# Kernel optimization log

Measured on AMD Instinct MI355X. Metric: run time of the kernel, lower is better.

The kernel has to match this reference:

```python
import jax, jax.numpy as jnp
import numpy as np

EPS = 1e-5
COORD_TAU, COORD_KAPPA = 1.0, 1.0
COT_TAU, COT_LAM = 0.8, 0.7
GATE_FLOOR = 0.05


def _gconv(x, w, b=None):
    # grouped 1x1 conv: x [B,C,H,W], w [g, co_per_g, ci_per_g]
    B, C, H, W = x.shape
    g, co, ci = w.shape
    y = jnp.einsum('goi,bgihw->bgohw', w, x.reshape(B, g, ci, H, W)).reshape(B, g * co, H, W)
    return y if b is None else y + b[None, :, None, None]


def _conv1x1(x, w):
    # dense 1x1 conv: w [Cout, Cin]
    return jnp.einsum('oi,bihw->bohw', w, x)


def _inorm(x, g, b):
    # InstanceNorm2d(affine=True): per (B,C) stats over spatial dims, biased var
    mu = x.mean(axis=(2, 3), keepdims=True)
    var = x.var(axis=(2, 3), keepdims=True)
    return (x - mu) * jax.lax.rsqrt(var + EPS) * g[None, :, None, None] + b[None, :, None, None]


def _axis_softmax(z, L, axis):
    # stabilized softmax along a spatial axis, mean-rescaled by L
    zz = z / COORD_TAU
    zz = zz - zz.max(axis=axis, keepdims=True)
    return jax.nn.softmax(zz, axis=axis) * L


def _forward(x, compress_w, inc_g, inc_b, coord_proj_w, coord_proj_g, coord_proj_b,
             coord_h_w, coord_h_b, coord_wc_w, coord_wc_b, coord_alpha, coord_beta,
             cot_key_w, cot_val_w, cot_att1_w, cot_attn_g, cot_attn_b, cot_att2_w,
             cot_fuse_w, fusion_w, fus_g, fus_b, gate_w, expand_w):
    xc = jax.nn.relu(_inorm(_conv1x1(x, compress_w), inc_g, inc_b))  # [B,m,H,W]
    B, C, H, W = xc.shape

    # ---- Coord2H branch (use_softmax=True path) ----
    def proj(t):
        return jax.nn.silu(_inorm(_gconv(t, coord_proj_w), coord_proj_g, coord_proj_b))

    zh = _gconv(proj(xc.mean(axis=3, keepdims=True)), coord_h_w, coord_h_b)   # [B,C,H,1]
    zw = _gconv(proj(xc.mean(axis=2, keepdims=True)), coord_wc_w, coord_wc_b)  # [B,C,1,W]
    ah = _axis_softmax(zh, H, 2)
    aw = _axis_softmax(zw, W, 3)
    w_lin = coord_alpha * ah + coord_beta * aw  # broadcasts to [B,C,H,W]
    coord_out = xc * (1.0 + COORD_KAPPA * (w_lin - 1.0))

    # ---- CoT branch ----
    k1 = _gconv(xc, cot_key_w)
    v = _gconv(xc, cot_val_w)
    y = jnp.concatenate([k1, xc], axis=1)  # [B,2C,H,W]
    att = jax.nn.relu(_inorm(_gconv(y, cot_att1_w), cot_attn_g, cot_attn_b))
    att_logits = _gconv(att, cot_att2_w)
    z = (att_logits / COT_TAU).reshape(B, C, H * W)
    sm = jax.nn.softmax(z - z.max(axis=-1, keepdims=True), axis=-1).reshape(B, C, H, W) * (H * W)
    att_mix = (1.0 - COT_LAM) * jax.nn.sigmoid(att_logits) + COT_LAM * sm
    cot_out = _conv1x1(k1 + att_mix * v, cot_fuse_w)

    # ---- fusion + gate + expand ----
    fused = jax.nn.relu(_inorm(_conv1x1(jnp.concatenate([coord_out, cot_out], axis=1), fusion_w), fus_g, fus_b))
    gate = jax.nn.sigmoid(jnp.einsum('oi,bi->bo', gate_w, fused.mean(axis=(2, 3))))[:, :, None, None]  # [B,1,1,1]
    return _conv1x1(fused * (gate * (1.0 - GATE_FLOOR) + GATE_FLOOR), expand_w)


def setup_inputs() -> dict:
    key = jax.random.key(0)
    B, DIM, H, W = 8, 512, 128, 128
    RED, G = 16, 4
    m = DIM // RED  # 32
    mg = m // G     # 8
    ks = jax.random.split(key, 23)

    def n(k, s, sc=0.05):
        return jax.random.normal(k, s, dtype=jnp.float32) * sc

    return {
        'x': jax.random.normal(ks[0], (B, DIM, H, W), dtype=jnp.float32),
        'compress_w': n(ks[1], (m, DIM)),
        'inc_g': 1.0 + n(ks[2], (m,)),
        'inc_b': n(ks[3], (m,)),
        'coord_proj_w': n(ks[4], (G, mg, mg), 0.2),
        'coord_proj_g': 1.0 + n(ks[5], (m,)),
        'coord_proj_b': n(ks[6], (m,)),
        'coord_h_w': n(ks[7], (G, mg, mg), 0.2),
        'coord_h_b': n(ks[8], (m,)),
        'coord_wc_w': n(ks[9], (G, mg, mg), 0.2),
        'coord_wc_b': n(ks[10], (m,)),
        'coord_alpha': jnp.asarray(0.5, dtype=jnp.float32),
        'coord_beta': jnp.asarray(0.5, dtype=jnp.float32),
        'cot_key_w': n(ks[11], (G, mg, mg), 0.2),
        'cot_val_w': n(ks[12], (G, mg, mg), 0.2),
        'cot_att1_w': n(ks[13], (G, mg, 2 * mg), 0.2),
        'cot_attn_g': 1.0 + n(ks[14], (m,)),
        'cot_attn_b': n(ks[15], (m,)),
        'cot_att2_w': n(ks[16], (G, mg, mg), 0.2),
        'cot_fuse_w': n(ks[17], (m, m), 0.1),
        'fusion_w': n(ks[18], (m, 2 * m), 0.1),
        'fus_g': 1.0 + n(ks[19], (m,)),
        'fus_b': n(ks[20], (m,)),
        'gate_w': n(ks[21], (1, m), 0.2),
        'expand_w': n(ks[22], (DIM, m), 0.1),
    }


def reference(x, compress_w, inc_g, inc_b, coord_proj_w, coord_proj_g, coord_proj_b,
              coord_h_w, coord_h_b, coord_wc_w, coord_wc_b, coord_alpha, coord_beta,
              cot_key_w, cot_val_w, cot_att1_w, cot_attn_g, cot_attn_b, cot_att2_w,
              cot_fuse_w, fusion_w, fus_g, fus_b, gate_w, expand_w):
    return _forward(x, compress_w, inc_g, inc_b, coord_proj_w, coord_proj_g, coord_proj_b,
                    coord_h_w, coord_h_b, coord_wc_w, coord_wc_b, coord_alpha, coord_beta,
                    cot_key_w, cot_val_w, cot_att1_w, cot_attn_g, cot_attn_b, cot_att2_w,
                    cot_fuse_w, fusion_w, fus_g, fus_b, gate_w, expand_w)
```

## Files before the change

### kernel.cpp

```cpp
#include <hip/hip_runtime.h>
#include <math.h>

#define NB 8
#define CIN 512
#define CM 32
#define MG 8
#define HH 128
#define WW 128
#define HWSZ (HH*WW)
#define EPSF 1e-5f
#define COT_ITAU 1.25f
#define LAM 0.7f
#define GFLOOR 0.05f

typedef float vf4 __attribute__((ext_vector_type(4)));

__device__ __forceinline__ float wsum(float v){
#pragma unroll
  for (int o = 32; o; o >>= 1) v += __shfl_xor(v, o, 64);
  return v;
}

__global__ void k_tw(const float* __restrict__ w, float* __restrict__ wT){
  int i = blockIdx.x*256 + threadIdx.x;
  if (i < CM*CIN){
    int c = i >> 9, k = i & (CIN-1);
    wT[k*CM + c] = w[i];
  }
}

__global__ __launch_bounds__(256) void k_compress(
    const float* __restrict__ x, const float* __restrict__ wT,
    float* __restrict__ y, float* __restrict__ s1, float* __restrict__ s2)
{
  int tid = threadIdx.x;
  int b = blockIdx.x >> 6;
  int p = ((blockIdx.x & 63) << 8) + tid;
  const float* xb = x + ((size_t)b*CIN)*HWSZ + p;
  float acc[CM];
#pragma unroll
  for (int c=0;c<CM;c++) acc[c]=0.f;
  float xv[8], xn[8];
#pragma unroll
  for (int u=0;u<8;u++) xv[u] = __builtin_nontemporal_load(&xb[(size_t)u*HWSZ]);
  for (int i=0;i<CIN;i+=8){
    if (i+8<CIN){
#pragma unroll
      for (int u=0;u<8;u++) xn[u] = __builtin_nontemporal_load(&xb[(size_t)(i+8+u)*HWSZ]);
    }
#pragma unroll
    for (int u=0;u<8;u++){
      const float* wr = wT + (i+u)*CM;
#pragma unroll
      for (int c=0;c<CM;c++) acc[c]=fmaf(wr[c],xv[u],acc[c]);
    }
#pragma unroll
    for (int u=0;u<8;u++) xv[u]=xn[u];
  }
  float* yb = y + ((size_t)b*CM)*HWSZ + p;
#pragma unroll
  for (int c=0;c<CM;c++) yb[(size_t)c*HWSZ] = acc[c];
  float ms=0.f, mq=0.f;
#pragma unroll
  for (int c=0;c<CM;c++){
    float s = wsum(acc[c]);
    float q = wsum(acc[c]*acc[c]);
    if ((tid&63)==c){ ms=s; mq=q; }
  }
  int lane = tid & 63;
  if (lane < CM){
    atomicAdd(&s1[b*CM+lane], ms);
    atomicAdd(&s2[b*CM+lane], mq);
  }
}

__global__ __launch_bounds__(256) void k_poolstat(
  const float* __restrict__ y,
  const float* __restrict__ s1i, const float* __restrict__ s2i,
  const float* __restrict__ incg, const float* __restrict__ incb,
  const float* __restrict__ kw, const float* __restrict__ a1w,
  float* __restrict__ s1, float* __restrict__ s2,
  float* __restrict__ hpool, float* __restrict__ wpart)
{
  __shared__ float nA[CM], nB[CM];
  __shared__ float sh[CM][128];
  int tid=threadIdx.x;
  int blk=blockIdx.x;
  int b = blk >> 6;
  int p = ((blk&63)<<8)+tid;
  if (tid<CM){
    float mu  = s1i[b*CM+tid]*(1.f/HWSZ);
    float var = fmaf(-mu,mu, s2i[b*CM+tid]*(1.f/HWSZ));
    float a   = rsqrtf(var+EPSF)*incg[tid];
    nA[tid]=a; nB[tid]=incb[tid]-mu*a;
  }
  __syncthreads();
  size_t base = ((size_t)b*CM)*HWSZ + p;
  float xc[CM], k1[CM], at[CM];
#pragma unroll
  for (int c=0;c<CM;c++)
    xc[c] = fmaxf(0.f, fmaf(y[base+(size_t)c*HWSZ], nA[c], nB[c]));
  if (tid>=128){
#pragma unroll
    for (int c=0;c<CM;c++) sh[c][tid-128]=xc[c];
  }
  __syncthreads();
  if (tid<128){
    float* wp = wpart + (size_t)blk*(CM*WW) + tid;
#pragma unroll
    for (int c=0;c<CM;c++) wp[c*WW] = xc[c] + sh[c][tid];
  }
  {
    int hrow = p >> 7;
    float ms=0.f;
#pragma unroll
    for (int c=0;c<CM;c++){
      float s=wsum(xc[c]);
      if ((tid&63)==c) ms=s;
    }
    int lane=tid&63;
    if (lane<CM) atomicAdd(&hpool[(b*CM+lane)*HH+hrow], ms*(1.f/WW));
  }
#pragma unroll
  for (int gI=0;gI<4;gI++)
#pragma unroll
    for (int o=0;o<MG;o++){
      float sk=0.f;
#pragma unroll
      for (int i=0;i<MG;i++) sk = fmaf(kw[gI*64+o*8+i], xc[gI*MG+i], sk);
      k1[gI*MG+o]=sk;
    }
#pragma unroll
  for (int gI=0;gI<4;gI++)
#pragma unroll
    for (int o=0;o<MG;o++){
      float s=0.f;
#pragma unroll
      for (int i=0;i<16;i++){
        float inp = (gI<2) ? k1[gI*16+i] : xc[(gI-2)*16+i];
        s = fmaf(a1w[gI*128+o*16+i], inp, s);
      }
      at[gI*MG+o]=s;
    }
  float ms=0.f,mq=0.f;
#pragma unroll
  for (int c=0;c<CM;c++){
    float s=wsum(at[c]); float q=wsum(at[c]*at[c]);
    if ((tid&63)==c){ms=s;mq=q;}
  }
  int lane=tid&63;
  if (lane<CM){ atomicAdd(&s1[b*CM+lane],ms); atomicAdd(&s2[b*CM+lane],mq); }
}

__global__ __launch_bounds__(256) void k_cot2(
  const float* __restrict__ y,
  const float* __restrict__ s1i, const float* __restrict__ s2i,
  const float* __restrict__ incg, const float* __restrict__ incb,
  const float* __restrict__ s1a, const float* __restrict__ s2a,
  const float* __restrict__ ag, const float* __restrict__ ab,
  const float* __restrict__ kw, const float* __restrict__ a1w, const float* __restrict__ a2w,
  const float* __restrict__ hpool, const float* __restrict__ wpart,
  const float* __restrict__ pjw, const float* __restrict__ pjg, const float* __restrict__ pjb,
  const float* __restrict__ chw, const float* __restrict__ chb,
  const float* __restrict__ cww, const float* __restrict__ cwb,
  float* __restrict__ es, float* __restrict__ ah, float* __restrict__ aw)
{
  __shared__ float T[CM][HH+1];
  __shared__ float sa[CM], sb[CM], smx[CM], ssc[CM];
  __shared__ float nA[CM], nB[CM], tA[CM], tB[CM];
  int tid=threadIdx.x;
  int blk=blockIdx.x;
  int b = blk >> 6;
  int p = ((blk&63)<<8)+tid;
  if (tid<CM){
    float mu  = s1i[b*CM+tid]*(1.f/HWSZ);
    float var = fmaf(-mu,mu, s2i[b*CM+tid]*(1.f/HWSZ));
    float a   = rsqrtf(var+EPSF)*incg[tid];
    nA[tid]=a; nB[tid]=incb[tid]-mu*a;
    float mu2  = s1a[b*CM+tid]*(1.f/HWSZ);
    float var2 = fmaf(-mu2,mu2, s2a[b*CM+tid]*(1.f/HWSZ));
    float a2   = rsqrtf(var2+EPSF)*ag[tid];
    tA[tid]=a2; tB[tid]=ab[tid]-mu2*a2;
  }
  __syncthreads();
  size_t base = ((size_t)b*CM)*HWSZ + p;
  float xc[CM], k1[CM], at[CM], l[CM];
#pragma unroll
  for (int c=0;c<CM;c++)
    xc[c] = fmaxf(0.f, fmaf(y[base+(size_t)c*HWSZ], nA[c], nB[c]));
#pragma unroll
  for (int gI=0;gI<4;gI++)
#pragma unroll
    for (int o=0;o<MG;o++){
      float sk=0.f;
#pragma unroll
      for (int i=0;i<MG;i++) sk = fmaf(kw[gI*64+o*8+i], xc[gI*MG+i], sk);
      k1[gI*MG+o]=sk;
    }
#pragma unroll
  for (int gI=0;gI<4;gI++)
#pragma unroll
    for (int o=0;o<MG;o++){
      float s=0.f;
#pragma unroll
      for (int i=0;i<16;i++){
        float inp = (gI<2) ? k1[gI*16+i] : xc[(gI-2)*16+i];
        s = fmaf(a1w[gI*128+o*16+i], inp, s);
      }
      at[gI*MG+o]=s;
    }
#pragma unroll
  for (int c=0;c<CM;c++)
    at[c] = fmaxf(0.f, fmaf(at[c], tA[c], tB[c]));
#pragma unroll
  for (int gI=0;gI<4;gI++)
#pragma unroll
    for (int o=0;o<MG;o++){
      float s=0.f;
#pragma unroll
      for (int i=0;i<MG;i++) s = fmaf(a2w[gI*64+o*8+i], at[gI*8+i], s);
      l[gI*MG+o]=s;
    }
  float ms=0.f;
#pragma unroll
  for (int c=0;c<CM;c++){
    float s = wsum(__expf(l[c]*COT_ITAU));
    if ((tid&63)==c) ms=s;
  }
  int lane=tid&63;
  if (lane<CM) atomicAdd(&es[b*CM+lane], ms);

  if (blk < 2*NB){
    int bb = blk>>1, path = blk&1;
    const float* w2 = path ? cww : chw;
    const float* b2 = path ? cwb : chb;
    float* outp     = path ? aw  : ah;
    float in[CM];
    if (path==1){
      __syncthreads();
      for (int t=tid; t<CM*WW; t+=256){
        const float* src = wpart + (size_t)(bb*64)*(CM*WW) + t;
        float s=0.f;
#pragma unroll 8
        for (int k=0;k<64;k++) s += src[(size_t)k*(CM*WW)];
        T[t>>7][t&127] = s*(1.f/HH);
      }
      __syncthreads();
      if (tid<HH){
#pragma unroll
        for (int c=0;c<CM;c++) in[c]=T[c][tid];
      }
      __syncthreads();
    } else {
      if (tid<HH){
#pragma unroll
        for (int c=0;c<CM;c++) in[c]=hpool[(bb*CM+c)*HH+tid];
      }
      __syncthreads();
    }
    if (tid<HH){
#pragma unroll
      for (int gI=0;gI<4;gI++)
#pragma unroll
        for (int o=0;o<MG;o++){
          float s=0.f;
#pragma unroll
          for (int i=0;i<MG;i++) s = fmaf(pjw[gI*64+o*8+i], in[gI*8+i], s);
          T[gI*8+o][tid] = s;
        }
    }
    __syncthreads();
    if (tid < CM){
      float s=0.f, q=0.f;
      for (int k=0;k<HH;k++){ float t=T[tid][k]; s+=t; q+=t*t; }
      float mu = s*(1.0f/HH);
      float var = q*(1.0f/HH) - mu*mu;
      float a = rsqrtf(var+EPSF)*pjg[tid];
      sa[tid]=a; sb[tid]=pjb[tid]-mu*a;
    }
    __syncthreads();
    float z[CM];
    if (tid<HH){
      float sil[CM];
#pragma unroll
      for (int c=0;c<CM;c++){
        float val = fmaf(T[c][tid], sa[c], sb[c]);
        sil[c] = val/(1.f+__expf(-val));
      }
#pragma unroll
      for (int gI=0;gI<4;gI++)
#pragma unroll
        for (int o=0;o<MG;o++){
          float s=b2[gI*8+o];
#pragma unroll
          for (int i=0;i<MG;i++) s = fmaf(w2[gI*64+o*8+i], sil[gI*8+i], s);
          z[gI*8+o]=s;
        }
    }
    __syncthreads();
    if (tid<HH){
#pragma unroll
      for (int c=0;c<CM;c++) T[c][tid]=z[c];
    }
    __syncthreads();
    if (tid < CM){
      float mx=-1e30f;
      for (int k=0;k<HH;k++) mx = fmaxf(mx, T[tid][k]);
      float s=0.f;
      for (int k=0;k<HH;k++) s += __expf(T[tid][k]-mx);
      smx[tid]=mx; ssc[tid]=(float)HH/s;
    }
    __syncthreads();
    if (tid<HH){
#pragma unroll
      for (int c=0;c<CM;c++)
        outp[(bb*CM+c)*HH + tid] = __expf(T[c][tid]-smx[c])*ssc[c];
    }
  }
}

__global__ __launch_bounds__(256) void k_mix_fuse(
  const float* __restrict__ y,
  const float* __restrict__ s1i, const float* __restrict__ s2i,
  const float* __restrict__ incg, const float* __restrict__ incb,
  const float* __restrict__ s1a, const float* __restrict__ s2a,
  const float* __restrict__ ag, const float* __restrict__ ab,
  const float* __restrict__ kw, const float* __restrict__ vw,
  const float* __restrict__ a1w, const float* __restrict__ a2w,
  const float* __restrict__ ah, const float* __restrict__ awp, const float* __restrict__ es,
  const float* __restrict__ alpha, const float* __restrict__ beta,
  const float* __restrict__ fw, const float* __restrict__ fuw,
  float* __restrict__ fpo, float* __restrict__ s1, float* __restrict__ s2)
{
  __shared__ float nA[CM], nB[CM], tA[CM], tB[CM];
  int tid=threadIdx.x;
  int b = blockIdx.x>>6;
  int p = ((blockIdx.x&63)<<8)+tid;
  int h = p >> 7, w = p & (WW-1);
  if (tid<CM){
    float mu  = s1i[b*CM+tid]*(1.f/HWSZ);
    float var = fmaf(-mu,mu, s2i[b*CM+tid]*(1.f/HWSZ));
    float a   = rsqrtf(var+EPSF)*incg[tid];
    nA[tid]=a; nB[tid]=incb[tid]-mu*a;
    float mu2  = s1a[b*CM+tid]*(1.f/HWSZ);
    float var2 = fmaf(-mu2,mu2, s2a[b*CM+tid]*(1.f/HWSZ));
    float a2   = rsqrtf(var2+EPSF)*ag[tid];
    tA[tid]=a2; tB[tid]=ab[tid]-mu2*a2;
  }
  __syncthreads();
  size_t base = ((size_t)b*CM)*HWSZ + p;
  float al=alpha[0], be=beta[0];
  float xc[CM], k1[CM], at[CM], l[CM], t[CM];
#pragma unroll
  for (int c=0;c<CM;c++)
    xc[c] = fmaxf(0.f, fmaf(y[base+(size_t)c*HWSZ], nA[c], nB[c]));
#pragma unroll
  for (int gI=0;gI<4;gI++)
#pragma unroll
    for (int o=0;o<MG;o++){
      float sk=0.f;
#pragma unroll
      for (int i=0;i<MG;i++) sk = fmaf(kw[gI*64+o*8+i], xc[gI*MG+i], sk);
      k1[gI*MG+o]=sk;
    }
#pragma unroll
  for (int gI=0;gI<4;gI++)
#pragma unroll
    for (int o=0;o<MG;o++){
      float s=0.f;
#pragma unroll
      for (int i=0;i<16;i++){
        float inp = (gI<2) ? k1[gI*16+i] : xc[(gI-2)*16+i];
        s = fmaf(a1w[gI*128+o*16+i], inp, s);
      }
      at[gI*MG+o]=s;
    }
#pragma unroll
  for (int c=0;c<CM;c++)
    at[c] = fmaxf(0.f, fmaf(at[c], tA[c], tB[c]));
#pragma unroll
  for (int gI=0;gI<4;gI++)
#pragma unroll
    for (int o=0;o<MG;o++){
      float s=0.f;
#pragma unroll
      for (int i=0;i<MG;i++) s = fmaf(a2w[gI*64+o*8+i], at[gI*8+i], s);
      l[gI*MG+o]=s;
    }
#pragma unroll
  for (int gI=0;gI<4;gI++)
#pragma unroll
    for (int o=0;o<MG;o++){
      float sv=0.f;
#pragma unroll
      for (int i=0;i<MG;i++) sv = fmaf(vw[gI*64+o*8+i], xc[gI*MG+i], sv);
      int c = gI*MG+o;
      float lgv = l[c];
      float sm = __expf(lgv*COT_ITAU) * (16384.f/es[b*CM+c]);
      float sg = 1.f/(1.f+__expf(-lgv));
      float mix = (1.f-LAM)*sg + LAM*sm;
      t[c] = fmaf(mix, sv, k1[c]);
    }
  float co[CM];
#pragma unroll
  for (int c=0;c<CM;c++){
    float wl = al*ah[(b*CM+c)*HH + h] + be*awp[(b*CM+c)*WW + w];
    co[c] = xc[c] * wl;
  }
  float cot[CM];
#pragma unroll
  for (int o=0;o<CM;o++){
    float s=0.f;
#pragma unroll
    for (int i=0;i<CM;i++) s = fmaf(fw[o*CM+i], t[i], s);
    cot[o]=s;
  }
  float ms=0.f, mq=0.f;
#pragma unroll
  for (int o=0;o<CM;o++){
    float s=0.f;
#pragma unroll
    for (int i=0;i<CM;i++) s = fmaf(fuw[o*64+i], co[i], s);
#pragma unroll
    for (int i=0;i<CM;i++) s = fmaf(fuw[o*64+32+i], cot[i], s);
    fpo[base+(size_t)o*HWSZ]=s;
    float ss = wsum(s); float qq = wsum(s*s);
    if ((tid&63)==o){ ms=ss; mq=qq; }
  }
  int lane=tid&63;
  if (lane<CM){ atomicAdd(&s1[b*CM+lane],ms); atomicAdd(&s2[b*CM+lane],mq); }
}

__global__ __launch_bounds__(256) void k_gstat(const float4* __restrict__ fp,
  const float* __restrict__ s1f, const float* __restrict__ s2f,
  const float* __restrict__ fg, const float* __restrict__ fb,
  float* __restrict__ gsum)
{
  int idx = blockIdx.x*256+threadIdx.x;
  int bc = idx >> 12;
  int c = bc & (CM-1);
  float mu  = s1f[bc]*(1.f/HWSZ);
  float var = fmaf(-mu,mu, s2f[bc]*(1.f/HWSZ));
  float a   = rsqrtf(var+EPSF)*fg[c];
  float bb  = fb[c]-mu*a;
  float4 tv = fp[idx];
  float s = fmaxf(0.f,fmaf(tv.x,a,bb))+fmaxf(0.f,fmaf(tv.y,a,bb))
          + fmaxf(0.f,fmaf(tv.z,a,bb))+fmaxf(0.f,fmaf(tv.w,a,bb));
  s = wsum(s);
  if ((threadIdx.x&63)==0) atomicAdd(&gsum[bc], s);
}

__global__ __launch_bounds__(256) void k_expand(const float4* __restrict__ fp4,
  const float* __restrict__ s1f, const float* __restrict__ s2f,
  const float* __restrict__ fg, const float* __restrict__ fb,
  const float* __restrict__ gw, const float* __restrict__ gsum,
  const float* __restrict__ ew, vf4* __restrict__ out4)
{
  __shared__ float fA[CM], fB[CM];
  int tid = threadIdx.x;
  int b = blockIdx.x >> 4;
  int tile = blockIdx.x & 15;
  int p4 = tile*256 + tid;
  int og = blockIdx.y * 64;
  if (tid<CM){
    float mu  = s1f[b*CM+tid]*(1.f/HWSZ);
    float var = fmaf(-mu,mu, s2f[b*CM+tid]*(1.f/HWSZ));
    float a   = rsqrtf(var+EPSF)*fg[tid];
    fA[tid]=a; fB[tid]=fb[tid]-mu*a;
  }
  float s=0.f;
#pragma unroll
  for (int c=0;c<CM;c++) s = fmaf(gw[c], gsum[b*CM+c], s);
  s *= (1.0f/HWSZ);
  float gt = 1.f/(1.f+__expf(-s));
  float sc = gt*(1.f-GFLOOR)+GFLOOR;
  __syncthreads();
  float4 f[CM];
  const float4* fbp = fp4 + ((size_t)b*CM)*(HWSZ/4) + p4;
#pragma unroll
  for (int c=0;c<CM;c++){
    float4 t = fbp[(size_t)c*(HWSZ/4)];
    float a=fA[c], bb=fB[c];
    f[c].x = fmaxf(0.f, fmaf(t.x,a,bb))*sc;
    f[c].y = fmaxf(0.f, fmaf(t.y,a,bb))*sc;
    f[c].z = fmaxf(0.f, fmaf(t.z,a,bb))*sc;
    f[c].w = fmaxf(0.f, fmaf(t.w,a,bb))*sc;
  }
  vf4* ob = out4 + ((size_t)b*CIN + og)*(HWSZ/4) + p4;
  for (int j=0;j<64;j++){
    const float* wr = ew + (og+j)*CM;
    vf4 acc = (vf4)(0.f);
#pragma unroll
    for (int c=0;c<CM;c++){
      float wv = wr[c];
      acc.x = fmaf(wv, f[c].x, acc.x);
      acc.y = fmaf(wv, f[c].y, acc.y);
      acc.z = fmaf(wv, f[c].z, acc.z);
      acc.w = fmaf(wv, f[c].w, acc.w);
    }
    __builtin_nontemporal_store(acc, &ob[(size_t)j*(HWSZ/4)]);
  }
}

extern "C" void kernel_launch(void* const* d_in, const int* in_sizes, int n_in,
                              void* d_out, int out_size, void* d_ws, size_t ws_size,
                              hipStream_t stream)
{
  const float* x    = (const float*)d_in[0];
  const float* cw   = (const float*)d_in[1];
  const float* incg = (const float*)d_in[2];
  const float* incb = (const float*)d_in[3];
  const float* pjw  = (const float*)d_in[4];
  const float* pjg  = (const float*)d_in[5];
  const float* pjb  = (const float*)d_in[6];
  const float* chw  = (const float*)d_in[7];
  const float* chb  = (const float*)d_in[8];
  const float* cww  = (const float*)d_in[9];
  const float* cwb  = (const float*)d_in[10];
  const float* alpha= (const float*)d_in[11];
  const float* beta = (const float*)d_in[12];
  const float* kw   = (const float*)d_in[13];
  const float* vw   = (const float*)d_in[14];
  const float* a1w  = (const float*)d_in[15];
  const float* ag   = (const float*)d_in[16];
  const float* ab   = (const float*)d_in[17];
  const float* a2w  = (const float*)d_in[18];
  const float* fw   = (const float*)d_in[19];
  const float* fuw  = (const float*)d_in[20];
  const float* fg   = (const float*)d_in[21];
  const float* fb   = (const float*)d_in[22];
  const float* gw   = (const float*)d_in[23];
  const float* ew   = (const float*)d_in[24];
  float* out = (float*)d_out;

  float* ws = (float*)d_ws;
  const size_t BIG = (size_t)NB*CM*HWSZ;
  float* y    = ws;
  float* F    = ws +   BIG;
  float* sm   = ws + 2*BIG;
  float* acc   = sm;  sm += 2048;
  float* statS = acc,      *statQ = acc+256;
  float* attS  = acc+512,  *attQ  = acc+768;
  float* esum  = acc+1024;
  float* fusS  = acc+1280, *fusQ  = acc+1536;
  float* gsum  = acc+1792;
  float* hpool = sm;  sm += NB*CM*HH;
  float* wT    = sm;  sm += CM*CIN;
  float* wpart = sm;  sm += (size_t)512*CM*WW;
  float* ahB   = sm;  sm += NB*CM*HH;
  float* awB   = sm;  sm += NB*CM*WW;

  hipMemsetAsync(acc, 0, (2048 + NB*CM*HH)*sizeof(float), stream);
  k_tw<<<64,256,0,stream>>>(cw, wT);
  k_compress<<<512,256,0,stream>>>(x, wT, y, statS, statQ);
  k_poolstat<<<512,256,0,stream>>>(y,statS,statQ,incg,incb,kw,a1w,attS,attQ,hpool,wpart);
  k_cot2<<<512,256,0,stream>>>(y,statS,statQ,incg,incb,attS,attQ,ag,ab,kw,a1w,a2w,
                               hpool,wpart,pjw,pjg,pjb,chw,chb,cww,cwb,esum,ahB,awB);
  k_mix_fuse<<<512,256,0,stream>>>(y,statS,statQ,incg,incb,attS,attQ,ag,ab,kw,vw,a1w,a2w,
                                   ahB,awB,esum,alpha,beta,fw,fuw,F,fusS,fusQ);
  k_gstat<<<4096,256,0,stream>>>((const float4*)F,fusS,fusQ,fg,fb,gsum);
  k_expand<<<dim3(128,8),256,0,stream>>>((const float4*)F,fusS,fusQ,fg,fb,gw,gsum,ew,(vf4*)out);
}
```

Baseline: 397.6 us.

## Split compress GEMM over input-channel groups with vectorized loads and separate reductions

The compress 1x1 conv is split into four input-channel groups (512 blocks in a 2D grid), each thread handling four pixels with float4 loads and writing partial sums to a workspace. A separate combine kernel sums the partials, writes y and accumulates the instance-norm statistics. The width-pool reduction is moved out of the two k_cot2 blocks into its own kernel. This aims for more memory-level parallelism and wider loads, at the cost of writing and re-reading four full-size partial tensors and two extra launches.

```diff
diff --git a/kernel.cpp b/kernel.cpp
--- a/kernel.cpp
+++ b/kernel.cpp
@@ -29,49 +29,61 @@
   }
 }
 
-__global__ __launch_bounds__(256) void k_compress(
+__global__ __launch_bounds__(256) void k_compress4(
     const float* __restrict__ x, const float* __restrict__ wT,
-    float* __restrict__ y, float* __restrict__ s1, float* __restrict__ s2)
+    float* __restrict__ part)
 {
   int tid = threadIdx.x;
-  int b = blockIdx.x >> 6;
-  int p = ((blockIdx.x & 63) << 8) + tid;
-  const float* xb = x + ((size_t)b*CIN)*HWSZ + p;
-  float acc[CM];
-#pragma unroll
-  for (int c=0;c<CM;c++) acc[c]=0.f;
-  float xv[8], xn[8];
-#pragma unroll
-  for (int u=0;u<8;u++) xv[u] = __builtin_nontemporal_load(&xb[(size_t)u*HWSZ]);
-  for (int i=0;i<CIN;i+=8){
-    if (i+8<CIN){
-#pragma unroll
-      for (int u=0;u<8;u++) xn[u] = __builtin_nontemporal_load(&xb[(size_t)(i+8+u)*HWSZ]);
-    }
-#pragma unroll
-    for (int u=0;u<8;u++){
-      const float* wr = wT + (i+u)*CM;
-#pragma unroll
-      for (int c=0;c<CM;c++) acc[c]=fmaf(wr[c],xv[u],acc[c]);
-    }
-#pragma unroll
-    for (int u=0;u<8;u++) xv[u]=xn[u];
-  }
-  float* yb = y + ((size_t)b*CM)*HWSZ + p;
-#pragma unroll
-  for (int c=0;c<CM;c++) yb[(size_t)c*HWSZ] = acc[c];
-  float ms=0.f, mq=0.f;
-#pragma unroll
-  for (int c=0;c<CM;c++){
-    float s = wsum(acc[c]);
-    float q = wsum(acc[c]*acc[c]);
-    if ((tid&63)==c){ ms=s; mq=q; }
-  }
-  int lane = tid & 63;
-  if (lane < CM){
-    atomicAdd(&s1[b*CM+lane], ms);
-    atomicAdd(&s2[b*CM+lane], mq);
-  }
+  int bt  = blockIdx.x;
+  int kg  = blockIdx.y;
+  int b   = bt >> 4;
+  int p4  = (bt & 15)*256 + tid;
+  const vf4* xb = (const vf4*)(x + ((size_t)b*CIN + kg*128)*HWSZ) + p4;
+  const float* wh = wT + kg*128*CM;
+  vf4 acc[CM];
+#pragma unroll
+  for (int c=0;c<CM;c++) acc[c] = (vf4)(0.f);
+  vf4 xv[4], xn[4];
+#pragma unroll
+  for (int u=0;u<4;u++) xv[u] = __builtin_nontemporal_load(xb + (size_t)u*(HWSZ/4));
+  for (int i=0;i<128;i+=4){
+    if (i+4<128){
+#pragma unroll
+      for (int u=0;u<4;u++) xn[u] = __builtin_nontemporal_load(xb + (size_t)(i+4+u)*(HWSZ/4));
+    }
+#pragma unroll
+    for (int u=0;u<4;u++){
+      const float* wr = wh + (i+u)*CM;
+#pragma unroll
+      for (int c=0;c<CM;c++){
+        float wv = wr[c];
+        acc[c].x = fmaf(wv, xv[u].x, acc[c].x);
+        acc[c].y = fmaf(wv, xv[u].y, acc[c].y);
+        acc[c].z = fmaf(wv, xv[u].z, acc[c].z);
+        acc[c].w = fmaf(wv, xv[u].w, acc[c].w);
+      }
+    }
+#pragma unroll
+    for (int u=0;u<4;u++) xv[u]=xn[u];
+  }
+  vf4* ob = (vf4*)(part + (size_t)kg*NB*CM*HWSZ) + (size_t)(b*CM)*(HWSZ/4) + p4;
+#pragma unroll
+  for (int c=0;c<CM;c++) ob[(size_t)c*(HWSZ/4)] = acc[c];
+}
+
+__global__ __launch_bounds__(256) void k_comb4(
+    const vf4* __restrict__ p0, const vf4* __restrict__ p1,
+    const vf4* __restrict__ p2, const vf4* __restrict__ p3,
+    vf4* __restrict__ y, float* __restrict__ s1, float* __restrict__ s2)
+{
+  int idx = blockIdx.x*256 + threadIdx.x;
+  vf4 a = p0[idx] + p1[idx] + p2[idx] + p3[idx];
+  y[idx] = a;
+  int bc = idx >> 12;
+  float s = a.x+a.y+a.z+a.w;
+  float q = a.x*a.x+a.y*a.y+a.z*a.z+a.w*a.w;
+  s = wsum(s); q = wsum(q);
+  if ((threadIdx.x&63)==0){ atomicAdd(&s1[bc],s); atomicAdd(&s2[bc],q); }
 }
 
 __global__ __launch_bounds__(256) void k_poolstat(
@@ -152,6 +164,18 @@
   if (lane<CM){ atomicAdd(&s1[b*CM+lane],ms); atomicAdd(&s2[b*CM+lane],mq); }
 }
 
+__global__ void k_wred(const float* __restrict__ wpart, float* __restrict__ wpool){
+  int bc = blockIdx.x;
+  int w  = threadIdx.x;
+  int b  = bc >> 5;
+  int c  = bc & 31;
+  const float* src = wpart + (size_t)(b*64)*(CM*WW) + c*WW + w;
+  float s=0.f;
+#pragma unroll 8
+  for (int k=0;k<64;k++) s += src[(size_t)k*(CM*WW)];
+  wpool[bc*WW + w] = s*(1.0f/HH);
+}
+
 __global__ __launch_bounds__(256) void k_cot2(
   const float* __restrict__ y,
   const float* __restrict__ s1i, const float* __restrict__ s2i,
@@ -159,7 +183,7 @@
   const float* __restrict__ s1a, const float* __restrict__ s2a,
   const float* __restrict__ ag, const float* __restrict__ ab,
   const float* __restrict__ kw, const float* __restrict__ a1w, const float* __restrict__ a2w,
-  const float* __restrict__ hpool, const float* __restrict__ wpart,
+  const float* __restrict__ hpool, const float* __restrict__ wpool,
   const float* __restrict__ pjw, const float* __restrict__ pjg, const float* __restrict__ pjb,
   const float* __restrict__ chw, const float* __restrict__ chb,
   const float* __restrict__ cww, const float* __restrict__ cwb,
@@ -232,33 +256,15 @@
 
   if (blk < 2*NB){
     int bb = blk>>1, path = blk&1;
-    const float* w2 = path ? cww : chw;
-    const float* b2 = path ? cwb : chb;
-    float* outp     = path ? aw  : ah;
-    float in[CM];
-    if (path==1){
-      __syncthreads();
-      for (int t=tid; t<CM*WW; t+=256){
-        const float* src = wpart + (size_t)(bb*64)*(CM*WW) + t;
-        float s=0.f;
-#pragma unroll 8
-        for (int k=0;k<64;k++) s += src[(size_t)k*(CM*WW)];
-        T[t>>7][t&127] = s*(1.f/HH);
-      }
-      __syncthreads();
-      if (tid<HH){
-#pragma unroll
-        for (int c=0;c<CM;c++) in[c]=T[c][tid];
-      }
-      __syncthreads();
-    } else {
-      if (tid<HH){
-#pragma unroll
-        for (int c=0;c<CM;c++) in[c]=hpool[(bb*CM+c)*HH+tid];
-      }
-      __syncthreads();
-    }
+    const float* pool = path ? wpool : hpool;
+    const float* w2   = path ? cww : chw;
+    const float* b2   = path ? cwb : chb;
+    float* outp       = path ? aw  : ah;
+    float z[CM];
     if (tid<HH){
+      float in[CM];
+#pragma unroll
+      for (int c=0;c<CM;c++) in[c] = pool[(bb*CM+c)*HH + tid];
 #pragma unroll
       for (int gI=0;gI<4;gI++)
 #pragma unroll
@@ -279,7 +285,6 @@
       sa[tid]=a; sb[tid]=pjb[tid]-mu*a;
     }
     __syncthreads();
-    float z[CM];
     if (tid<HH){
       float sil[CM];
 #pragma unroll
@@ -535,9 +540,10 @@
 
   float* ws = (float*)d_ws;
   const size_t BIG = (size_t)NB*CM*HWSZ;
-  float* y    = ws;
-  float* F    = ws +   BIG;
-  float* sm   = ws + 2*BIG;
+  float* part = ws;
+  float* F    = ws;
+  float* y    = ws + 4*BIG;
+  float* sm   = ws + 5*BIG;
   float* acc   = sm;  sm += 2048;
   float* statS = acc,      *statQ = acc+256;
   float* attS  = acc+512,  *attQ  = acc+768;
@@ -547,15 +553,20 @@
   float* hpool = sm;  sm += NB*CM*HH;
   float* wT    = sm;  sm += CM*CIN;
   float* wpart = sm;  sm += (size_t)512*CM*WW;
+  float* wpool = sm;  sm += NB*CM*WW;
   float* ahB   = sm;  sm += NB*CM*HH;
   float* awB   = sm;  sm += NB*CM*WW;
 
   hipMemsetAsync(acc, 0, (2048 + NB*CM*HH)*sizeof(float), stream);
   k_tw<<<64,256,0,stream>>>(cw, wT);
-  k_compress<<<512,256,0,stream>>>(x, wT, y, statS, statQ);
+  k_compress4<<<dim3(128,4),256,0,stream>>>(x, wT, part);
+  k_comb4<<<4096,256,0,stream>>>((const vf4*)part,(const vf4*)(part+BIG),
+                                 (const vf4*)(part+2*BIG),(const vf4*)(part+3*BIG),
+                                 (vf4*)y, statS, statQ);
   k_poolstat<<<512,256,0,stream>>>(y,statS,statQ,incg,incb,kw,a1w,attS,attQ,hpool,wpart);
+  k_wred<<<NB*CM,128,0,stream>>>(wpart, wpool);
   k_cot2<<<512,256,0,stream>>>(y,statS,statQ,incg,incb,attS,attQ,ag,ab,kw,a1w,a2w,
-                               hpool,wpart,pjw,pjg,pjb,chw,chb,cww,cwb,esum,ahB,awB);
+                               hpool,wpool,pjw,pjg,pjb,chw,chb,cww,cwb,esum,ahB,awB);
   k_mix_fuse<<<512,256,0,stream>>>(y,statS,statQ,incg,incb,attS,attQ,ag,ab,kw,vw,a1w,a2w,
                                    ahB,awB,esum,alpha,beta,fw,fuw,F,fusS,fusQ);
   k_gstat<<<4096,256,0,stream>>>((const float4*)F,fusS,fusQ,fg,fb,gsum);
```

Result: faster. 368.0 us (-7.5%).

## Stage compress input through double-buffered LDS and split W-pool reduction kernel

Applied to the files above, without the earlier changes.

The compress kernel now loads 32-channel slabs of x as float4 vectors into a double-buffered shared-memory tile, prefetching the next slab while computing. Results are also written back through LDS with vectorized stores. Separately, the W-axis pooling reduction moves out of two k_cot2 blocks into a dedicated small kernel, so those blocks no longer serialize a long reduction. This adds 64KB of LDS per block, which may lower occupancy, plus one extra launch.

```diff
diff --git a/kernel.cpp b/kernel.cpp
--- a/kernel.cpp
+++ b/kernel.cpp
@@ -33,44 +33,81 @@
     const float* __restrict__ x, const float* __restrict__ wT,
     float* __restrict__ y, float* __restrict__ s1, float* __restrict__ s2)
 {
+  __shared__ float lds[2][CM][256];
   int tid = threadIdx.x;
-  int b = blockIdx.x >> 6;
-  int p = ((blockIdx.x & 63) << 8) + tid;
-  const float* xb = x + ((size_t)b*CIN)*HWSZ + p;
+  int b   = blockIdx.x >> 6;
+  int tile0 = (blockIdx.x & 63) << 8;
+  const float* xb = x + ((size_t)b*CIN)*HWSZ + tile0;
+
+  {
+    const vf4* src = (const vf4*)xb;
+    vf4 tmp[8];
+#pragma unroll
+    for (int j=0;j<8;j++){
+      int f = tid + 256*j;
+      tmp[j] = __builtin_nontemporal_load(src + (size_t)(f>>6)*(HWSZ/4) + (f&63));
+    }
+#pragma unroll
+    for (int j=0;j<8;j++){
+      int f = tid + 256*j;
+      *((vf4*)&lds[0][f>>6][(f&63)*4]) = tmp[j];
+    }
+  }
   float acc[CM];
 #pragma unroll
   for (int c=0;c<CM;c++) acc[c]=0.f;
-  float xv[8], xn[8];
-#pragma unroll
-  for (int u=0;u<8;u++) xv[u] = __builtin_nontemporal_load(&xb[(size_t)u*HWSZ]);
-  for (int i=0;i<CIN;i+=8){
-    if (i+8<CIN){
-#pragma unroll
-      for (int u=0;u<8;u++) xn[u] = __builtin_nontemporal_load(&xb[(size_t)(i+8+u)*HWSZ]);
-    }
-#pragma unroll
-    for (int u=0;u<8;u++){
-      const float* wr = wT + (i+u)*CM;
-#pragma unroll
-      for (int c=0;c<CM;c++) acc[c]=fmaf(wr[c],xv[u],acc[c]);
-    }
-#pragma unroll
-    for (int u=0;u<8;u++) xv[u]=xn[u];
-  }
-  float* yb = y + ((size_t)b*CM)*HWSZ + p;
-#pragma unroll
-  for (int c=0;c<CM;c++) yb[(size_t)c*HWSZ] = acc[c];
-  float ms=0.f, mq=0.f;
-#pragma unroll
-  for (int c=0;c<CM;c++){
-    float s = wsum(acc[c]);
-    float q = wsum(acc[c]*acc[c]);
-    if ((tid&63)==c){ ms=s; mq=q; }
-  }
-  int lane = tid & 63;
-  if (lane < CM){
-    atomicAdd(&s1[b*CM+lane], ms);
-    atomicAdd(&s2[b*CM+lane], mq);
+
+  for (int t=0; t<16; ++t){
+    int cur = t & 1;
+    __syncthreads();
+    if (t+1 < 16){
+      const vf4* src = (const vf4*)(xb + (size_t)(t+1)*CM*HWSZ);
+      vf4 tmp[8];
+#pragma unroll
+      for (int j=0;j<8;j++){
+        int f = tid + 256*j;
+        tmp[j] = __builtin_nontemporal_load(src + (size_t)(f>>6)*(HWSZ/4) + (f&63));
+      }
+#pragma unroll
+      for (int j=0;j<8;j++){
+        int f = tid + 256*j;
+        *((vf4*)&lds[cur^1][f>>6][(f&63)*4]) = tmp[j];
+      }
+    }
+    const float* wr0 = wT + t*CM*CM;
+#pragma unroll
+    for (int i=0;i<CM;i++){
+      float xv = lds[cur][i][tid];
+      const float* wr = wr0 + i*CM;
+#pragma unroll
+      for (int c=0;c<CM;c++) acc[c] = fmaf(wr[c], xv, acc[c]);
+    }
+  }
+  {
+    float ms=0.f, mq=0.f;
+#pragma unroll
+    for (int c=0;c<CM;c++){
+      float s = wsum(acc[c]);
+      float q = wsum(acc[c]*acc[c]);
+      if ((tid&63)==c){ ms=s; mq=q; }
+    }
+    int lane = tid & 63;
+    if (lane < CM){
+      atomicAdd(&s1[b*CM+lane], ms);
+      atomicAdd(&s2[b*CM+lane], mq);
+    }
+  }
+  __syncthreads();
+#pragma unroll
+  for (int c=0;c<CM;c++) lds[0][c][tid] = acc[c];
+  __syncthreads();
+  {
+    vf4* yb = (vf4*)(y + ((size_t)b*CM)*HWSZ + tile0);
+#pragma unroll
+    for (int j=0;j<8;j++){
+      int f = tid + 256*j;
+      yb[(size_t)(f>>6)*(HWSZ/4) + (f&63)] = *((vf4*)&lds[0][f>>6][(f&63)*4]);
+    }
   }
 }
 
@@ -152,6 +189,18 @@
   if (lane<CM){ atomicAdd(&s1[b*CM+lane],ms); atomicAdd(&s2[b*CM+lane],mq); }
 }
 
+__global__ void k_wred(const float* __restrict__ wpart, float* __restrict__ wpool){
+  int bc = blockIdx.x;
+  int w  = threadIdx.x;
+  int b  = bc >> 5;
+  int c  = bc & 31;
+  const float* src = wpart + (size_t)(b*64)*(CM*WW) + c*WW + w;
+  float s=0.f;
+#pragma unroll 8
+  for (int k=0;k<64;k++) s += src[(size_t)k*(CM*WW)];
+  wpool[bc*WW + w] = s*(1.0f/HH);
+}
+
 __global__ __launch_bounds__(256) void k_cot2(
   const float* __restrict__ y,
   const float* __restrict__ s1i, const float* __restrict__ s2i,
@@ -159,7 +208,7 @@
   const float* __restrict__ s1a, const float* __restrict__ s2a,
   const float* __restrict__ ag, const float* __restrict__ ab,
   const float* __restrict__ kw, const float* __restrict__ a1w, const float* __restrict__ a2w,
-  const float* __restrict__ hpool, const float* __restrict__ wpart,
+  const float* __restrict__ hpool, const float* __restrict__ wpool,
   const float* __restrict__ pjw, const float* __restrict__ pjg, const float* __restrict__ pjb,
   const float* __restrict__ chw, const float* __restrict__ chb,
   const float* __restrict__ cww, const float* __restrict__ cwb,
@@ -232,33 +281,15 @@
 
   if (blk < 2*NB){
     int bb = blk>>1, path = blk&1;
-    const float* w2 = path ? cww : chw;
-    const float* b2 = path ? cwb : chb;
-    float* outp     = path ? aw  : ah;
-    float in[CM];
-    if (path==1){
-      __syncthreads();
-      for (int t=tid; t<CM*WW; t+=256){
-        const float* src = wpart + (size_t)(bb*64)*(CM*WW) + t;
-        float s=0.f;
-#pragma unroll 8
-        for (int k=0;k<64;k++) s += src[(size_t)k*(CM*WW)];
-        T[t>>7][t&127] = s*(1.f/HH);
-      }
-      __syncthreads();
-      if (tid<HH){
-#pragma unroll
-        for (int c=0;c<CM;c++) in[c]=T[c][tid];
-      }
-      __syncthreads();
-    } else {
-      if (tid<HH){
-#pragma unroll
-        for (int c=0;c<CM;c++) in[c]=hpool[(bb*CM+c)*HH+tid];
-      }
-      __syncthreads();
-    }
+    const float* pool = path ? wpool : hpool;
+    const float* w2   = path ? cww : chw;
+    const float* b2   = path ? cwb : chb;
+    float* outp       = path ? aw  : ah;
+    float z[CM];
     if (tid<HH){
+      float in[CM];
+#pragma unroll
+      for (int c=0;c<CM;c++) in[c] = pool[(bb*CM+c)*HH + tid];
 #pragma unroll
       for (int gI=0;gI<4;gI++)
 #pragma unroll
@@ -279,7 +310,6 @@
       sa[tid]=a; sb[tid]=pjb[tid]-mu*a;
     }
     __syncthreads();
-    float z[CM];
     if (tid<HH){
       float sil[CM];
 #pragma unroll
@@ -547,6 +577,7 @@
   float* hpool = sm;  sm += NB*CM*HH;
   float* wT    = sm;  sm += CM*CIN;
   float* wpart = sm;  sm += (size_t)512*CM*WW;
+  float* wpool = sm;  sm += NB*CM*WW;
   float* ahB   = sm;  sm += NB*CM*HH;
   float* awB   = sm;  sm += NB*CM*WW;
 
@@ -554,8 +585,9 @@
   k_tw<<<64,256,0,stream>>>(cw, wT);
   k_compress<<<512,256,0,stream>>>(x, wT, y, statS, statQ);
   k_poolstat<<<512,256,0,stream>>>(y,statS,statQ,incg,incb,kw,a1w,attS,attQ,hpool,wpart);
+  k_wred<<<NB*CM,128,0,stream>>>(wpart, wpool);
   k_cot2<<<512,256,0,stream>>>(y,statS,statQ,incg,incb,attS,attQ,ag,ab,kw,a1w,a2w,
-                               hpool,wpart,pjw,pjg,pjb,chw,chb,cww,cwb,esum,ahB,awB);
+                               hpool,wpool,pjw,pjg,pjb,chw,chb,cww,cwb,esum,ahB,awB);
   k_mix_fuse<<<512,256,0,stream>>>(y,statS,statQ,incg,incb,attS,attQ,ag,ab,kw,vw,a1w,a2w,
                                    ahB,awB,esum,alpha,beta,fw,fuw,F,fusS,fusQ);
   k_gstat<<<4096,256,0,stream>>>((const float4*)F,fusS,fusQ,fg,fb,gsum);
```

After: 376.8 us. 1.06x faster.

## Split compress reduction over four waves and move W-pool reduction to its own kernel

Applied to the files above, without the earlier changes.

The compress GEMM now gives each block a 64-pixel tile and splits the 512 input channels across four waves. Partial sums are reduced through shared memory, which quadruples the grid to 2048 blocks for better occupancy and latency hiding. Stores become vectorized float4 writes, and stats are reduced per channel. Separately, the W-direction pooling reduction that serially ran inside 8 blocks of k_cot2 is moved to a dedicated k_wred kernel with 256 blocks, removing a serial tail at the cost of an extra launch and workspace buffer.

```diff
diff --git a/kernel.cpp b/kernel.cpp
--- a/kernel.cpp
+++ b/kernel.cpp
@@ -33,44 +33,66 @@
     const float* __restrict__ x, const float* __restrict__ wT,
     float* __restrict__ y, float* __restrict__ s1, float* __restrict__ s2)
 {
-  int tid = threadIdx.x;
-  int b = blockIdx.x >> 6;
-  int p = ((blockIdx.x & 63) << 8) + tid;
-  const float* xb = x + ((size_t)b*CIN)*HWSZ + p;
+  __shared__ float part[4][CM][64];
+  int tid  = threadIdx.x;
+  int lane = tid & 63;
+  int g    = tid >> 6;
+  int blk  = blockIdx.x;
+  int b    = blk >> 8;
+  int tile0 = (blk & 255) << 6;
+  const float* xb = x + ((size_t)b*CIN + g*128)*HWSZ + tile0 + lane;
+  const float* wh = wT + (g*128)*CM;
+
   float acc[CM];
 #pragma unroll
   for (int c=0;c<CM;c++) acc[c]=0.f;
   float xv[8], xn[8];
 #pragma unroll
   for (int u=0;u<8;u++) xv[u] = __builtin_nontemporal_load(&xb[(size_t)u*HWSZ]);
-  for (int i=0;i<CIN;i+=8){
-    if (i+8<CIN){
+  for (int i=0;i<128;i+=8){
+    if (i+8<128){
 #pragma unroll
       for (int u=0;u<8;u++) xn[u] = __builtin_nontemporal_load(&xb[(size_t)(i+8+u)*HWSZ]);
     }
 #pragma unroll
     for (int u=0;u<8;u++){
-      const float* wr = wT + (i+u)*CM;
+      const float* wr = wh + (i+u)*CM;
 #pragma unroll
       for (int c=0;c<CM;c++) acc[c]=fmaf(wr[c],xv[u],acc[c]);
     }
 #pragma unroll
     for (int u=0;u<8;u++) xv[u]=xn[u];
   }
-  float* yb = y + ((size_t)b*CM)*HWSZ + p;
-#pragma unroll
-  for (int c=0;c<CM;c++) yb[(size_t)c*HWSZ] = acc[c];
-  float ms=0.f, mq=0.f;
-#pragma unroll
-  for (int c=0;c<CM;c++){
-    float s = wsum(acc[c]);
-    float q = wsum(acc[c]*acc[c]);
-    if ((tid&63)==c){ ms=s; mq=q; }
-  }
-  int lane = tid & 63;
-  if (lane < CM){
-    atomicAdd(&s1[b*CM+lane], ms);
-    atomicAdd(&s2[b*CM+lane], mq);
+#pragma unroll
+  for (int c=0;c<CM;c++) part[g][c][lane]=acc[c];
+  __syncthreads();
+  {
+    int idx0 = tid*8;
+    int c = idx0>>6, p0 = idx0&63;
+    vf4 a0 = *((vf4*)&part[0][c][p0])   + *((vf4*)&part[1][c][p0])
+           + *((vf4*)&part[2][c][p0])   + *((vf4*)&part[3][c][p0]);
+    vf4 a1 = *((vf4*)&part[0][c][p0+4]) + *((vf4*)&part[1][c][p0+4])
+           + *((vf4*)&part[2][c][p0+4]) + *((vf4*)&part[3][c][p0+4]);
+    *((vf4*)&part[0][c][p0])   = a0;
+    *((vf4*)&part[0][c][p0+4]) = a1;
+  }
+  __syncthreads();
+#pragma unroll
+  for (int cc=0;cc<8;cc++){
+    int c = g*8+cc;
+    float v = part[0][c][lane];
+    float s = wsum(v);
+    float q = wsum(v*v);
+    if (lane==0){
+      atomicAdd(&s1[b*CM+c], s);
+      atomicAdd(&s2[b*CM+c], q);
+    }
+  }
+#pragma unroll
+  for (int k=0;k<2;k++){
+    int s = tid + 256*k;
+    int c = s>>4, p4 = (s&15)*4;
+    *((vf4*)(y + ((size_t)(b*CM+c))*HWSZ + tile0 + p4)) = *((vf4*)&part[0][c][p4]);
   }
 }
 
@@ -152,6 +174,18 @@
   if (lane<CM){ atomicAdd(&s1[b*CM+lane],ms); atomicAdd(&s2[b*CM+lane],mq); }
 }
 
+__global__ void k_wred(const float* __restrict__ wpart, float* __restrict__ wpool){
+  int bc = blockIdx.x;
+  int w  = threadIdx.x;
+  int b  = bc >> 5;
+  int c  = bc & 31;
+  const float* src = wpart + (size_t)(b*64)*(CM*WW) + c*WW + w;
+  float s=0.f;
+#pragma unroll 8
+  for (int k=0;k<64;k++) s += src[(size_t)k*(CM*WW)];
+  wpool[bc*WW + w] = s*(1.0f/HH);
+}
+
 __global__ __launch_bounds__(256) void k_cot2(
   const float* __restrict__ y,
   const float* __restrict__ s1i, const float* __restrict__ s2i,
@@ -159,7 +193,7 @@
   const float* __restrict__ s1a, const float* __restrict__ s2a,
   const float* __restrict__ ag, const float* __restrict__ ab,
   const float* __restrict__ kw, const float* __restrict__ a1w, const float* __restrict__ a2w,
-  const float* __restrict__ hpool, const float* __restrict__ wpart,
+  const float* __restrict__ hpool, const float* __restrict__ wpool,
   const float* __restrict__ pjw, const float* __restrict__ pjg, const float* __restrict__ pjb,
   const float* __restrict__ chw, const float* __restrict__ chb,
   const float* __restrict__ cww, const float* __restrict__ cwb,
@@ -232,33 +266,15 @@
 
   if (blk < 2*NB){
     int bb = blk>>1, path = blk&1;
-    const float* w2 = path ? cww : chw;
-    const float* b2 = path ? cwb : chb;
-    float* outp     = path ? aw  : ah;
-    float in[CM];
-    if (path==1){
-      __syncthreads();
-      for (int t=tid; t<CM*WW; t+=256){
-        const float* src = wpart + (size_t)(bb*64)*(CM*WW) + t;
-        float s=0.f;
-#pragma unroll 8
-        for (int k=0;k<64;k++) s += src[(size_t)k*(CM*WW)];
-        T[t>>7][t&127] = s*(1.f/HH);
-      }
-      __syncthreads();
-      if (tid<HH){
-#pragma unroll
-        for (int c=0;c<CM;c++) in[c]=T[c][tid];
-      }
-      __syncthreads();
-    } else {
-      if (tid<HH){
-#pragma unroll
-        for (int c=0;c<CM;c++) in[c]=hpool[(bb*CM+c)*HH+tid];
-      }
-      __syncthreads();
-    }
+    const float* pool = path ? wpool : hpool;
+    const float* w2   = path ? cww : chw;
+    const float* b2   = path ? cwb : chb;
+    float* outp       = path ? aw  : ah;
+    float z[CM];
     if (tid<HH){
+      float in[CM];
+#pragma unroll
+      for (int c=0;c<CM;c++) in[c] = pool[(bb*CM+c)*HH + tid];
 #pragma unroll
       for (int gI=0;gI<4;gI++)
 #pragma unroll
@@ -279,7 +295,6 @@
       sa[tid]=a; sb[tid]=pjb[tid]-mu*a;
     }
     __syncthreads();
-    float z[CM];
     if (tid<HH){
       float sil[CM];
 #pragma unroll
@@ -547,15 +562,17 @@
   float* hpool = sm;  sm += NB*CM*HH;
   float* wT    = sm;  sm += CM*CIN;
   float* wpart = sm;  sm += (size_t)512*CM*WW;
+  float* wpool = sm;  sm += NB*CM*WW;
   float* ahB   = sm;  sm += NB*CM*HH;
   float* awB   = sm;  sm += NB*CM*WW;
 
   hipMemsetAsync(acc, 0, (2048 + NB*CM*HH)*sizeof(float), stream);
   k_tw<<<64,256,0,stream>>>(cw, wT);
-  k_compress<<<512,256,0,stream>>>(x, wT, y, statS, statQ);
+  k_compress<<<2048,256,0,stream>>>(x, wT, y, statS, statQ);
   k_poolstat<<<512,256,0,stream>>>(y,statS,statQ,incg,incb,kw,a1w,attS,attQ,hpool,wpart);
+  k_wred<<<NB*CM,128,0,stream>>>(wpart, wpool);
   k_cot2<<<512,256,0,stream>>>(y,statS,statQ,incg,incb,attS,attQ,ag,ab,kw,a1w,a2w,
-                               hpool,wpart,pjw,pjg,pjb,chw,chb,cww,cwb,esum,ahB,awB);
+                               hpool,wpool,pjw,pjg,pjb,chw,chb,cww,cwb,esum,ahB,awB);
   k_mix_fuse<<<512,256,0,stream>>>(y,statS,statQ,incg,incb,attS,attQ,ag,ab,kw,vw,a1w,a2w,
                                    ahB,awB,esum,alpha,beta,fw,fuw,F,fusS,fusQ);
   k_gstat<<<4096,256,0,stream>>>((const float4*)F,fusS,fusQ,fg,fb,gsum);
```

After: 673.2 us. 1.69x slower.
